# Kernel optimization log

Hardware: AMD Instinct MI355X
Metric: run time of the kernel (lower is better)

The kernel has to match this reference:

```python
import jax, jax.numpy as jnp
import numpy as np

N_HEADS = 8
N_LSTM_LAYERS = 32
HID = 25  # LSTM hidden units == decoder seq_len
EPS = 1e-5


def _layernorm(x, g, b):
    m = x.mean(-1, keepdims=True)
    v = x.var(-1, keepdims=True)  # biased, as torch LayerNorm
    return (x - m) / jnp.sqrt(v + EPS) * g + b


def _mha(q_in, k_in, v_in, Wq, bq, Wk, bk, Wv, bv, Wo, bo):
    B, L, D = q_in.shape
    S = k_in.shape[1]
    E = D // N_HEADS
    q = (q_in @ Wq + bq).reshape(B, L, N_HEADS, E)
    k = (k_in @ Wk + bk).reshape(B, S, N_HEADS, E)
    v = (v_in @ Wv + bv).reshape(B, S, N_HEADS, E)
    scores = jnp.einsum('blhe,bshe->bhls', q, k) / jnp.sqrt(jnp.asarray(E, q.dtype))
    attn = jax.nn.softmax(scores, axis=-1)
    out = jnp.einsum('bhls,bshe->blhe', attn, v).reshape(B, L, D)
    return out @ Wo + bo


def _lstm_layer(inp, W_ih, W_hh, b_ih, b_hh):
    # inp: [B, T, F]; PyTorch gate order i, f, g, o
    B = inp.shape[0]
    h0 = jnp.zeros((B, HID), inp.dtype)
    c0 = jnp.zeros((B, HID), inp.dtype)
    bias = b_ih + b_hh

    def step(carry, x_t):
        h, c = carry
        gates = x_t @ W_ih.T + h @ W_hh.T + bias  # [B, 4H]
        i, f, g, o = jnp.split(gates, 4, axis=-1)
        c = jax.nn.sigmoid(f) * c + jax.nn.sigmoid(i) * jnp.tanh(g)
        h = jax.nn.sigmoid(o) * jnp.tanh(c)
        return (h, c), h

    xs = jnp.swapaxes(inp, 0, 1)  # [T, B, F]
    _, hs = jax.lax.scan(step, (h0, c0), xs)
    return jnp.swapaxes(hs, 0, 1)  # [B, T, H]


def _forward(x, cross,
             Wq_s, bq_s, Wk_s, bk_s, Wv_s, bv_s, Wo_s, bo_s,
             Wq_c, bq_c, Wk_c, bk_c, Wv_c, bv_c, Wo_c, bo_c,
             g1, b1, g2, b2, g3, b3,
             W_ih, W_hh, b_ih, b_hh, Wc, bc):
    x = x + _mha(x, x, x, Wq_s, bq_s, Wk_s, bk_s, Wv_s, bv_s, Wo_s, bo_s)
    x = _layernorm(x, g1, b1)
    x = x + _mha(x, cross, cross, Wq_c, bq_c, Wk_c, bk_c, Wv_c, bv_c, Wo_c, bo_c)
    x = _layernorm(x, g2, b2)
    # LSTM runs over the feature axis: [B, L=25, D=512] -> [B, T=512, F=25]
    y = jnp.swapaxes(x, 1, 2)
    for l in range(N_LSTM_LAYERS):
        y = _lstm_layer(y, W_ih[l], W_hh[l], b_ih[l], b_hh[l])
    # pointwise conv over channels (dim 1 of [B, 512, 25])
    final_y = jnp.einsum('oc,bcl->bol', Wc, y) + bc[None, :, None]
    final_y = jnp.swapaxes(final_y, 1, 2)  # [B, 25, 512]
    return _layernorm(x + final_y, g3, b3)


def setup_inputs() -> dict:
    key = jax.random.key(0)
    ks = jax.random.split(key, 24)
    B, L, S, D = 128, 25, 96, 512

    def rn(k, shape, scale=0.02):
        return jax.random.normal(k, shape, jnp.float32) * scale

    inp = {
        'x': jax.random.normal(ks[0], (B, L, D), jnp.float32),
        'cross': jax.random.normal(ks[1], (B, S, D), jnp.float32),
        'Wq_s': rn(ks[2], (D, D)), 'bq_s': jnp.zeros(D),
        'Wk_s': rn(ks[3], (D, D)), 'bk_s': jnp.zeros(D),
        'Wv_s': rn(ks[4], (D, D)), 'bv_s': jnp.zeros(D),
        'Wo_s': rn(ks[5], (D, D)), 'bo_s': jnp.zeros(D),
        'Wq_c': rn(ks[6], (D, D)), 'bq_c': jnp.zeros(D),
        'Wk_c': rn(ks[7], (D, D)), 'bk_c': jnp.zeros(D),
        'Wv_c': rn(ks[8], (D, D)), 'bv_c': jnp.zeros(D),
        'Wo_c': rn(ks[9], (D, D)), 'bo_c': jnp.zeros(D),
        'g1': jnp.ones(D), 'b1': jnp.zeros(D),
        'g2': jnp.ones(D), 'b2': jnp.zeros(D),
        'g3': jnp.ones(D), 'b3': jnp.zeros(D),
        'W_ih': rn(ks[10], (N_LSTM_LAYERS, 4 * HID, HID), 0.1),
        'W_hh': rn(ks[11], (N_LSTM_LAYERS, 4 * HID, HID), 0.1),
        'b_ih': jnp.zeros((N_LSTM_LAYERS, 4 * HID)),
        'b_hh': jnp.zeros((N_LSTM_LAYERS, 4 * HID)),
        'Wc': rn(ks[12], (D, D)), 'bc': jnp.zeros(D),
    }
    return inp


def reference(x, cross,
              Wq_s, bq_s, Wk_s, bk_s, Wv_s, bv_s, Wo_s, bo_s,
              Wq_c, bq_c, Wk_c, bk_c, Wv_c, bv_c, Wo_c, bo_c,
              g1, b1, g2, b2, g3, b3,
              W_ih, W_hh, b_ih, b_hh, Wc, bc):
    return _forward(x, cross,
                    Wq_s, bq_s, Wk_s, bk_s, Wv_s, bv_s, Wo_s, bo_s,
                    Wq_c, bq_c, Wk_c, bk_c, Wv_c, bv_c, Wo_c, bo_c,
                    g1, b1, g2, b2, g3, b3,
                    W_ih, W_hh, b_ih, b_hh, Wc, bc)
```

## Files before the change

### kernel.cpp

```cpp
#include <hip/hip_runtime.h>


#define EPS_LN 1e-5f

typedef _Float16 h2v __attribute__((ext_vector_type(2)));
typedef _Float16 h8v __attribute__((ext_vector_type(8)));
typedef float    f4v __attribute__((ext_vector_type(4)));

#if defined(__has_builtin)
#if __has_builtin(__builtin_amdgcn_fdot2)
#define HAVE_FDOT2 1
#endif
#if __has_builtin(__builtin_amdgcn_rcpf)
#define HAVE_RCPF 1
#endif
#endif

__device__ __forceinline__ float fdot2(h2v a, h2v b, float c) {
#ifdef HAVE_FDOT2
  return __builtin_amdgcn_fdot2(a, b, c, false);
#else
  return c + (float)a.x * (float)b.x + (float)a.y * (float)b.y;
#endif
}
__device__ __forceinline__ h2v bch2(unsigned int u) {
  return __builtin_bit_cast(h2v, u);
}
__device__ __forceinline__ float rcp_fast(float x) {
#ifdef HAVE_RCPF
  return __builtin_amdgcn_rcpf(x);
#else
  return 1.f / x;
#endif
}
__device__ __forceinline__ float sigm_fast(float x) {
  return rcp_fast(1.f + __expf(-x));
}
__device__ __forceinline__ float tanh_fast(float x) {
  return 1.f - 2.f * rcp_fast(1.f + __expf(2.f * x));
}

struct WPtrs { const float* p[9]; };

__global__ __launch_bounds__(256)
void prep_weights(WPtrs w, _Float16* __restrict__ dst) {
  __shared__ float tile[32][33];
  const int z = blockIdx.z;
  const int tx = threadIdx.x & 31, ty = threadIdx.x >> 5;
  const int bx = blockIdx.x, by = blockIdx.y;
  const float* in = w.p[z];
  _Float16* outp = dst + (size_t)z * 262144;
  if (z < 8) {
#pragma unroll
    for (int i = 0; i < 4; i++)
      tile[ty + i * 8][tx] = in[(size_t)(by * 32 + ty + i * 8) * 512 + bx * 32 + tx];
    __syncthreads();
#pragma unroll
    for (int i = 0; i < 4; i++)
      outp[(size_t)(bx * 32 + ty + i * 8) * 512 + by * 32 + tx] = (_Float16)tile[tx][ty + i * 8];
  } else {
#pragma unroll
    for (int i = 0; i < 4; i++) {
      size_t off = (size_t)(by * 32 + ty + i * 8) * 512 + bx * 32 + tx;
      outp[off] = (_Float16)in[off];
    }
  }
}

__global__ __launch_bounds__(256)
void gemm3(const float* __restrict__ A,
           const _Float16* __restrict__ BT0, const _Float16* __restrict__ BT1,
           const _Float16* __restrict__ BT2,
           const float* __restrict__ bias0, const float* __restrict__ bias1,
           const float* __restrict__ bias2,
           float* __restrict__ C0, float* __restrict__ C1, float* __restrict__ C2,
           int M) {
  __shared__ _Float16 Asld[64 * 40];
  __shared__ _Float16 Bsld[64 * 40];
  const int t = threadIdx.x;
  const int which = blockIdx.x >> 3;
  const int n0 = (blockIdx.x & 7) * 64;
  const int m0 = blockIdx.y * 64;
  const _Float16* BT = (which == 0) ? BT0 : (which == 1) ? BT1 : BT2;
  const float* bias  = (which == 0) ? bias0 : (which == 1) ? bias1 : bias2;
  float* C           = (which == 0) ? C0 : (which == 1) ? C1 : C2;

  const int r = t >> 2, q = t & 3;
  const int w = t >> 6;
  const int lane = t & 63;
  const int lm = lane & 15, q8 = lane >> 4;

  f4v acc[4] = {};
  for (int k0 = 0; k0 < 512; k0 += 32) {
    __syncthreads();
    float4 f0 = *(const float4*)&A[(size_t)(m0 + r) * 512 + k0 + q * 8];
    float4 f1 = *(const float4*)&A[(size_t)(m0 + r) * 512 + k0 + q * 8 + 4];
    h8v hvv = {(_Float16)f0.x, (_Float16)f0.y, (_Float16)f0.z, (_Float16)f0.w,
               (_Float16)f1.x, (_Float16)f1.y, (_Float16)f1.z, (_Float16)f1.w};
    *(h8v*)&Asld[r * 40 + q * 8] = hvv;
    *(uint4*)&Bsld[r * 40 + q * 8] = *(const uint4*)&BT[(size_t)(n0 + r) * 512 + k0 + q * 8];
    __syncthreads();
    h8v a = *(const h8v*)&Asld[(w * 16 + lm) * 40 + q8 * 8];
#pragma unroll
    for (int nt = 0; nt < 4; nt++) {
      h8v b = *(const h8v*)&Bsld[(nt * 16 + lm) * 40 + q8 * 8];
      acc[nt] = __builtin_amdgcn_mfma_f32_16x16x32_f16(a, b, acc[nt], 0, 0, 0);
    }
  }
#pragma unroll
  for (int nt = 0; nt < 4; nt++) {
    int gn = n0 + nt * 16 + lm;
    float bv = bias[gn];
#pragma unroll
    for (int rg = 0; rg < 4; rg++) {
      int gm = m0 + w * 16 + q8 * 4 + rg;
      C[(size_t)gm * 512 + gn] = acc[nt][rg] + bv;
    }
  }
}

template <int S>
__global__ __launch_bounds__(256)
void attn_scores(const float* __restrict__ Q, const float* __restrict__ K,
                 float* __restrict__ P) {
  __shared__ float Qs[25][64];
  __shared__ float Ks[S][65];
  const int h = blockIdx.x, b = blockIdx.y, t = threadIdx.x;
  for (int idx = t; idx < 25 * 64; idx += 256) {
    int l = idx >> 6, e = idx & 63;
    Qs[l][e] = Q[(b * 25 + l) * 512 + h * 64 + e];
  }
  for (int idx = t; idx < S * 64; idx += 256) {
    int s = idx >> 6, e = idx & 63;
    Ks[s][e] = K[(b * S + s) * 512 + h * 64 + e];
  }
  __syncthreads();
  float* Pb = P + (size_t)(b * 8 + h) * 25 * S;
  for (int idx = t; idx < 25 * S; idx += 256) {
    int l = idx / S, s = idx % S;
    float acc = 0.f;
#pragma unroll
    for (int e = 0; e < 64; e++) acc += Qs[l][e] * Ks[s][e];
    Pb[idx] = acc * 0.125f;
  }
}

template <int S>
__global__ __launch_bounds__(256)
void attn_out(const float* __restrict__ P, const float* __restrict__ V,
              float* __restrict__ O) {
  __shared__ float Ps[25][S];
  __shared__ float Vs[S][64];
  const int h = blockIdx.x, b = blockIdx.y, t = threadIdx.x;
  const float* Pb = P + (size_t)(b * 8 + h) * 25 * S;
  for (int idx = t; idx < 25 * S; idx += 256) Ps[idx / S][idx % S] = Pb[idx];
  for (int idx = t; idx < S * 64; idx += 256) {
    int s = idx >> 6, e = idx & 63;
    Vs[s][e] = V[(b * S + s) * 512 + h * 64 + e];
  }
  __syncthreads();
  if (t < 25) {
    float mx = -1e30f;
    for (int s = 0; s < S; s++) mx = fmaxf(mx, Ps[t][s]);
    float sum = 0.f;
    for (int s = 0; s < S; s++) { float p = __expf(Ps[t][s] - mx); Ps[t][s] = p; sum += p; }
    float r = 1.f / sum;
    for (int s = 0; s < S; s++) Ps[t][s] *= r;
  }
  __syncthreads();
  for (int idx = t; idx < 25 * 64; idx += 256) {
    int l = idx >> 6, e = idx & 63;
    float acc = 0.f;
    for (int s = 0; s < S; s++) acc += Ps[l][s] * Vs[s][e];
    O[(b * 25 + l) * 512 + h * 64 + e] = acc;
  }
}

__global__ __launch_bounds__(128)
void add_ln(const float* __restrict__ a, const float* __restrict__ b,
            const float* __restrict__ gw, const float* __restrict__ bw,
            float* __restrict__ out) {
  const int row = blockIdx.x, t = threadIdx.x;
  float4 va = ((const float4*)(a + (size_t)row * 512))[t];
  float4 vb = ((const float4*)(b + (size_t)row * 512))[t];
  float4 v = make_float4(va.x + vb.x, va.y + vb.y, va.z + vb.z, va.w + vb.w);
  float s = v.x + v.y + v.z + v.w;
  float q = v.x * v.x + v.y * v.y + v.z * v.z + v.w * v.w;
#pragma unroll
  for (int off = 32; off > 0; off >>= 1) {
    s += __shfl_down(s, off);
    q += __shfl_down(q, off);
  }
  __shared__ float red[4];
  if ((t & 63) == 0) { red[(t >> 6) * 2] = s; red[(t >> 6) * 2 + 1] = q; }
  __syncthreads();
  float S_ = red[0] + red[2], Q_ = red[1] + red[3];
  float mean = S_ * (1.f / 512.f);
  float var  = Q_ * (1.f / 512.f) - mean * mean;
  float inv  = rsqrtf(var + EPS_LN);
  float4 g4 = ((const float4*)gw)[t];
  float4 b4 = ((const float4*)bw)[t];
  float4 o;
  o.x = (v.x - mean) * inv * g4.x + b4.x;
  o.y = (v.y - mean) * inv * g4.y + b4.y;
  o.z = (v.z - mean) * inv * g4.z + b4.z;
  o.w = (v.w - mean) * inv * g4.w + b4.w;
  ((float4*)(out + (size_t)row * 512))[t] = o;
}

__global__ void transpose_dl(const float* __restrict__ in, float* __restrict__ outp) {
  const int b = blockIdx.x, t = threadIdx.x;
  for (int idx = t; idx < 25 * 512; idx += 256) {
    int l2 = idx / 512, c = idx % 512;
    outp[((size_t)b * 25 + l2) * 512 + c] = in[((size_t)b * 512 + c) * 25 + l2];
  }
}

__global__ __launch_bounds__(256)
void prep_x0r(const float* __restrict__ x2, _Float16* __restrict__ X0) {
  __shared__ float tile[25][516];
  const int b = blockIdx.x, t = threadIdx.x;
  for (int idx = t; idx < 25 * 512; idx += 256) {
    int u = idx >> 9, d = idx & 511;
    tile[u][d] = x2[((size_t)b * 25 + u) * 512 + d];
  }
  __syncthreads();
  for (int idx = t; idx < 512 * 32; idx += 256) {
    int d = idx >> 5, u = idx & 31;
    X0[((size_t)b * 512 + d) * 32 + u] = (u < 25) ? (_Float16)tile[u][d] : (_Float16)0.f;
  }
}

#define NLAY 32
#define NGRP 16
#define BGRP 8
#define NPIPE 64
#define CHT  8
#define NCHK 64
#define RSLOTS 64
#define RCHK (RSLOTS / CHT)
#define RLAY ((size_t)128 * RSLOTS * 32)

__device__ __forceinline__ int ld_rlx(int* p) {
  return __hip_atomic_load(p, __ATOMIC_RELAXED, __HIP_MEMORY_SCOPE_AGENT);
}
__device__ __forceinline__ void st_rlx(int* p, int v) {
  __hip_atomic_store(p, v, __ATOMIC_RELAXED, __HIP_MEMORY_SCOPE_AGENT);
}
__device__ __forceinline__ unsigned long long ldq_rlx(const unsigned long long* p) {
  return __hip_atomic_load(p, __ATOMIC_RELAXED, __HIP_MEMORY_SCOPE_AGENT);
}
__device__ __forceinline__ void sth_rlx(_Float16* p, _Float16 v) {
  __hip_atomic_store((unsigned short*)p, __builtin_bit_cast(unsigned short, v),
                     __ATOMIC_RELAXED, __HIP_MEMORY_SCOPE_AGENT);
}

__global__ __launch_bounds__(256) __attribute__((amdgpu_waves_per_eu(2, 2)))
void lstm_pipeline(const _Float16* __restrict__ X0, float* __restrict__ yout,
                   _Float16* __restrict__ ring, int* __restrict__ prod,
                   int* __restrict__ cons,
                   const float* __restrict__ Wih, const float* __restrict__ Whh,
                   const float* __restrict__ bih, const float* __restrict__ bhh) {
  const int l = blockIdx.x / NGRP;
  const int g = blockIdx.x % NGRP;
  const int t = threadIdx.x;
  const int lane = t & 63;
  const int wv = t >> 6;
  const int u  = t & 31;
  const int bi = t >> 5;
  const int p  = g * 4 + wv;
  const bool active = (u < 25);

  __shared__ _Float16 xbuf[CHT][BGRP][32];
  __shared__ _Float16 hbuf[BGRP][32];

  h2v wih2[4][13], whh2[4][13];
  float bias_r[4];
  float c_reg = 0.f;
  {
    const int uc = active ? u : 24;
#pragma unroll
    for (int j = 0; j < 4; j++) {
      const float* wi = &Wih[((size_t)l * 100 + j * 25 + uc) * 25];
      const float* wh = &Whh[((size_t)l * 100 + j * 25 + uc) * 25];
#pragma unroll
      for (int k = 0; k < 13; k++) {
        float alo = wi[2 * k], ahi = (2 * k + 1 < 25) ? wi[2 * k + 1] : 0.f;
        float blo = wh[2 * k], bhi = (2 * k + 1 < 25) ? wh[2 * k + 1] : 0.f;
        wih2[j][k] = h2v{(_Float16)alo, (_Float16)ahi};
        whh2[j][k] = h2v{(_Float16)blo, (_Float16)bhi};
      }
      bias_r[j] = bih[l * 100 + j * 25 + uc] + bhh[l * 100 + j * 25 + uc];
    }
  }
  hbuf[2 * wv + (lane >> 5)][lane & 31] = (_Float16)0.f;

  _Float16* ring_out = ring + (size_t)l * RLAY
                       + ((size_t)(g * BGRP + bi) * RSLOTS) * 32 + u;
  float* yout_out = yout + ((size_t)(g * BGRP + bi) * 512) * 25 + u;

  const int s_tc = lane >> 3;
  const int s_b2 = 2 * wv + ((lane >> 2) & 1);
  const int s_seg = lane & 3;

  int* prod_in   = prod + (l - 1) * NPIPE + p;
  int* prod_out  = prod + l * NPIPE + p;
  int* cons_self = cons + l * NPIPE + p;
  int* cons_up   = cons + (l + 1) * NPIPE + p;

  for (int n = 0; n < NCHK; n++) {
    if (l > 0) {
      while (ld_rlx(prod_in) < n + 1) __builtin_amdgcn_s_sleep(1);
    }
    if (l < NLAY - 1 && n >= RCHK) {
      while (ld_rlx(cons_up) < n - RCHK + 1) __builtin_amdgcn_s_sleep(1);
    }
    asm volatile("" ::: "memory");

    {
      const int tg = n * CHT + s_tc;
      if (l == 0) {
        const uint4* p4 = (const uint4*)(X0
            + (((size_t)(g * BGRP + s_b2) * 512) + tg) * 32 + s_seg * 8);
        *(uint4*)&xbuf[s_tc][s_b2][s_seg * 8] = *p4;
      } else {
        const unsigned long long* p8 = (const unsigned long long*)(ring
            + (size_t)(l - 1) * RLAY
            + (((size_t)(g * BGRP + s_b2) * RSLOTS) + (tg & (RSLOTS - 1))) * 32
            + s_seg * 8);
        unsigned long long a = ldq_rlx(p8);
        unsigned long long b = ldq_rlx(p8 + 1);
        *(uint4*)&xbuf[s_tc][s_b2][s_seg * 8] =
            make_uint4((unsigned)a, (unsigned)(a >> 32),
                       (unsigned)b, (unsigned)(b >> 32));
      }
    }
    asm volatile("s_waitcnt lgkmcnt(0)" ::: "memory");
    if (lane == 0 && l > 0) st_rlx(cons_self, n + 1);

    float ax[CHT][4];
    if (active) {
#pragma unroll
      for (int tc = 0; tc < CHT; tc++) {
        const unsigned int* xr = (const unsigned int*)&xbuf[tc][bi][0];
        uint4 xa = *(const uint4*)(xr);
        uint4 xb = *(const uint4*)(xr + 4);
        uint4 xc = *(const uint4*)(xr + 8);
        unsigned int xd = xr[12];
        h2v xk[13] = {bch2(xa.x), bch2(xa.y), bch2(xa.z), bch2(xa.w),
                      bch2(xb.x), bch2(xb.y), bch2(xb.z), bch2(xb.w),
                      bch2(xc.x), bch2(xc.y), bch2(xc.z), bch2(xc.w),
                      bch2(xd)};
        float a0 = bias_r[0], a1 = bias_r[1], a2 = bias_r[2], a3 = bias_r[3];
#pragma unroll
        for (int k = 0; k < 13; k++) {
          a0 = fdot2(wih2[0][k], xk[k], a0);
          a1 = fdot2(wih2[1][k], xk[k], a1);
          a2 = fdot2(wih2[2][k], xk[k], a2);
          a3 = fdot2(wih2[3][k], xk[k], a3);
        }
        ax[tc][0] = a0; ax[tc][1] = a1; ax[tc][2] = a2; ax[tc][3] = a3;
      }
    }

#pragma unroll
    for (int tc = 0; tc < CHT; tc++) {
      const int tg = n * CHT + tc;
      if (active) {
        const unsigned int* hr = (const unsigned int*)&hbuf[bi][0];
        uint4 ha = *(const uint4*)(hr);
        uint4 hb = *(const uint4*)(hr + 4);
        uint4 hc = *(const uint4*)(hr + 8);
        unsigned int hd = hr[12];
        h2v hk[13] = {bch2(ha.x), bch2(ha.y), bch2(ha.z), bch2(ha.w),
                      bch2(hb.x), bch2(hb.y), bch2(hb.z), bch2(hb.w),
                      bch2(hc.x), bch2(hc.y), bch2(hc.z), bch2(hc.w),
                      bch2(hd)};
        float a0 = ax[tc][0], a1 = ax[tc][1], a2 = ax[tc][2], a3 = ax[tc][3];
#pragma unroll
        for (int k = 0; k < 13; k++) {
          a0 = fdot2(whh2[0][k], hk[k], a0);
          a1 = fdot2(whh2[1][k], hk[k], a1);
          a2 = fdot2(whh2[2][k], hk[k], a2);
          a3 = fdot2(whh2[3][k], hk[k], a3);
        }
        float si = sigm_fast(a0);
        float sf = sigm_fast(a1);
        float so = sigm_fast(a3);
        c_reg = sf * c_reg + si * tanh_fast(a2);
        float h = so * tanh_fast(c_reg);
        _Float16 h16 = (_Float16)h;
        hbuf[bi][u] = h16;
        if (l == NLAY - 1)
          yout_out[(size_t)tg * 25] = h;
        else
          sth_rlx(ring_out + (size_t)(tg & (RSLOTS - 1)) * 32, h16);
      }
    }
    asm volatile("s_waitcnt vmcnt(0)" ::: "memory");
    if (lane == 0 && l < NLAY - 1) st_rlx(prod_out, n + 1);
  }
}

extern "C" void kernel_launch(void* const* d_in, const int* in_sizes, int n_in,
                              void* d_out, int out_size, void* d_ws, size_t ws_size,
                              hipStream_t stream) {
  const float* x     = (const float*)d_in[0];
  const float* cross = (const float*)d_in[1];
  const float* Wq_s = (const float*)d_in[2];  const float* bq_s = (const float*)d_in[3];
  const float* Wk_s = (const float*)d_in[4];  const float* bk_s = (const float*)d_in[5];
  const float* Wv_s = (const float*)d_in[6];  const float* bv_s = (const float*)d_in[7];
  const float* Wo_s = (const float*)d_in[8];  const float* bo_s = (const float*)d_in[9];
  const float* Wq_c = (const float*)d_in[10]; const float* bq_c = (const float*)d_in[11];
  const float* Wk_c = (const float*)d_in[12]; const float* bk_c = (const float*)d_in[13];
  const float* Wv_c = (const float*)d_in[14]; const float* bv_c = (const float*)d_in[15];
  const float* Wo_c = (const float*)d_in[16]; const float* bo_c = (const float*)d_in[17];
  const float* g1 = (const float*)d_in[18]; const float* b1 = (const float*)d_in[19];
  const float* g2 = (const float*)d_in[20]; const float* b2 = (const float*)d_in[21];
  const float* g3 = (const float*)d_in[22]; const float* b3 = (const float*)d_in[23];
  const float* Wih = (const float*)d_in[24];
  const float* Whh = (const float*)d_in[25];
  const float* bih = (const float*)d_in[26];
  const float* bhh = (const float*)d_in[27];
  const float* Wc  = (const float*)d_in[28]; const float* bc = (const float*)d_in[29];
  float* out = (float*)d_out;
  float* ws  = (float*)d_ws;

  constexpr size_t A  = 1638400;
  constexpr size_t C6 = 6291456;
  float* x1    = ws;
  float* Qc    = ws + A;
  float* Qs    = ws + 2 * A;
  float* Ks    = ws + 3 * A;
  float* Vs    = ws + 4 * A;
  float* attns = ws + 5 * A;
  float* tmp   = ws + 6 * A;
  float* Ps    = ws + 7 * A;
  float* Kc    = ws + 2 * A;
  float* Vc    = ws + 2 * A + C6;
  float* attnc = ws + 2 * A + 2 * C6;
  float* Pc    = attnc + A;
  float* tmp2  = ws + 6 * A;
  float* x2    = ws + 3 * A;
  _Float16* X0b  = (_Float16*)(ws + 4 * A);
  float*    youtb = ws + 5 * A;
  _Float16* ringb = (_Float16*)(ws + 6 * A);
  float* ytb   = ws + 2 * A;
  float* fy    = ws + 5 * A;
  _Float16* WTall = (_Float16*)(ws + 20000000);
  int* ctr = (int*)(ws + 21179648);

  dim3 blk(256);
  WPtrs wpq;
  wpq.p[0] = Wq_s; wpq.p[1] = Wk_s; wpq.p[2] = Wv_s; wpq.p[3] = Wo_s;
  wpq.p[4] = Wq_c; wpq.p[5] = Wk_c; wpq.p[6] = Wv_c; wpq.p[7] = Wo_c;
  wpq.p[8] = Wc;
  prep_weights<<<dim3(16, 16, 9), blk, 0, stream>>>(wpq, WTall);
  hipMemsetAsync(ctr, 0, 4096 * sizeof(int), stream);
  _Float16* WT[9];
  for (int i = 0; i < 9; i++) WT[i] = WTall + (size_t)i * 262144;

  gemm3<<<dim3(24, 50), blk, 0, stream>>>(x, WT[0], WT[1], WT[2],
                                          bq_s, bk_s, bv_s, Qs, Ks, Vs, 3200);
  attn_scores<25><<<dim3(8, 128), blk, 0, stream>>>(Qs, Ks, Ps);
  attn_out<25><<<dim3(8, 128), blk, 0, stream>>>(Ps, Vs, attns);
  gemm3<<<dim3(8, 50), blk, 0, stream>>>(attns, WT[3], WT[3], WT[3],
                                         bo_s, bo_s, bo_s, tmp, tmp, tmp, 3200);
  add_ln<<<3200, 128, 0, stream>>>(x, tmp, g1, b1, x1);
  gemm3<<<dim3(8, 50), blk, 0, stream>>>(x1, WT[4], WT[4], WT[4],
                                         bq_c, bq_c, bq_c, Qc, Qc, Qc, 3200);
  gemm3<<<dim3(16, 192), blk, 0, stream>>>(cross, WT[5], WT[6], WT[6],
                                           bk_c, bv_c, bv_c, Kc, Vc, Vc, 12288);
  attn_scores<96><<<dim3(8, 128), blk, 0, stream>>>(Qc, Kc, Pc);
  attn_out<96><<<dim3(8, 128), blk, 0, stream>>>(Pc, Vc, attnc);
  gemm3<<<dim3(8, 50), blk, 0, stream>>>(attnc, WT[7], WT[7], WT[7],
                                         bo_c, bo_c, bo_c, tmp2, tmp2, tmp2, 3200);
  add_ln<<<3200, 128, 0, stream>>>(x1, tmp2, g2, b2, x2);
  prep_x0r<<<128, 256, 0, stream>>>(x2, X0b);
  lstm_pipeline<<<NLAY * NGRP, 256, 0, stream>>>(X0b, youtb, ringb, ctr, ctr + 2048,
                                                 Wih, Whh, bih, bhh);
  transpose_dl<<<128, 256, 0, stream>>>(youtb, ytb);
  gemm3<<<dim3(8, 50), blk, 0, stream>>>(ytb, WT[8], WT[8], WT[8],
                                         bc, bc, bc, fy, fy, fy, 3200);
  add_ln<<<3200, 128, 0, stream>>>(x2, fy, g3, b3, out);
}
```

Measured before the change: 912.3 us.

## Remap LSTM pipeline so a block's waves hold consecutive layers, handing off via LDS

Each block of the layer-pipelined LSTM used to hold one layer for 8 batch rows, with every layer-to-layer handoff going through a global ring buffer and agent-scope atomic counters. Now each block holds 4 consecutive layers (one per wave) for 2 batch rows. Inside a block, hidden states pass through an LDS ring with LDS producer/consumer counters, so global ring traffic and global polling only happen at boundaries between blocks of 4 layers. This cuts global memory latency on the pipeline's critical path. In exchange it adds intra-block spin-waiting on LDS counters and a 4-slot LDS buffer that could stall waves.

```diff
diff --git a/kernel.cpp b/kernel.cpp
--- a/kernel.cpp
+++ b/kernel.cpp
@@ -232,11 +232,12 @@
 }
 
 #define NLAY 32
-#define NGRP 16
-#define BGRP 8
+#define LGRP 8
+#define WPB  4
 #define NPIPE 64
 #define CHT  8
 #define NCHK 64
+#define NSLOT 4
 #define RSLOTS 64
 #define RCHK (RSLOTS / CHT)
 #define RLAY ((size_t)128 * RSLOTS * 32)
@@ -253,6 +254,12 @@
 __device__ __forceinline__ void sth_rlx(_Float16* p, _Float16 v) {
   __hip_atomic_store((unsigned short*)p, __builtin_bit_cast(unsigned short, v),
                      __ATOMIC_RELAXED, __HIP_MEMORY_SCOPE_AGENT);
+}
+__device__ __forceinline__ int ld_lds(int* p) {
+  return __hip_atomic_load(p, __ATOMIC_RELAXED, __HIP_MEMORY_SCOPE_WORKGROUP);
+}
+__device__ __forceinline__ void st_lds(int* p, int v) {
+  __hip_atomic_store(p, v, __ATOMIC_RELAXED, __HIP_MEMORY_SCOPE_WORKGROUP);
 }
 
 __global__ __launch_bounds__(256) __attribute__((amdgpu_waves_per_eu(2, 2)))
@@ -261,18 +268,29 @@
                    int* __restrict__ cons,
                    const float* __restrict__ Wih, const float* __restrict__ Whh,
                    const float* __restrict__ bih, const float* __restrict__ bhh) {
-  const int l = blockIdx.x / NGRP;
-  const int g = blockIdx.x % NGRP;
+  const int lg = blockIdx.x / NPIPE;
+  const int p  = blockIdx.x % NPIPE;
   const int t = threadIdx.x;
   const int lane = t & 63;
   const int wv = t >> 6;
-  const int u  = t & 31;
-  const int bi = t >> 5;
-  const int p  = g * 4 + wv;
+  const int l  = lg * WPB + wv;
+  const int u  = lane & 31;
+  const int bi = lane >> 5;
   const bool active = (u < 25);
 
-  __shared__ _Float16 xbuf[CHT][BGRP][32];
-  __shared__ _Float16 hbuf[BGRP][32];
+  __shared__ _Float16 lbuf[3][NSLOT][CHT][2][32];
+  __shared__ _Float16 inbuf[CHT][2][32];
+  __shared__ _Float16 hbuf[WPB][2][32];
+  __shared__ int lprod[3], lcons[3];
+
+  for (int idx = t; idx < 3 * NSLOT * CHT * 2 * 32; idx += 256)
+    ((_Float16*)lbuf)[idx] = (_Float16)0.f;
+  for (int idx = t; idx < CHT * 2 * 32; idx += 256)
+    ((_Float16*)inbuf)[idx] = (_Float16)0.f;
+  for (int idx = t; idx < WPB * 2 * 32; idx += 256)
+    ((_Float16*)hbuf)[idx] = (_Float16)0.f;
+  if (t < 3) { lprod[t] = 0; lcons[t] = 0; }
+  __syncthreads();
 
   h2v wih2[4][13], whh2[4][13];
   float bias_r[4];
@@ -293,56 +311,64 @@
       bias_r[j] = bih[l * 100 + j * 25 + uc] + bhh[l * 100 + j * 25 + uc];
     }
   }
-  hbuf[2 * wv + (lane >> 5)][lane & 31] = (_Float16)0.f;
-
-  _Float16* ring_out = ring + (size_t)l * RLAY
-                       + ((size_t)(g * BGRP + bi) * RSLOTS) * 32 + u;
-  float* yout_out = yout + ((size_t)(g * BGRP + bi) * 512) * 25 + u;
-
-  const int s_tc = lane >> 3;
-  const int s_b2 = 2 * wv + ((lane >> 2) & 1);
-  const int s_seg = lane & 3;
-
-  int* prod_in   = prod + (l - 1) * NPIPE + p;
-  int* prod_out  = prod + l * NPIPE + p;
-  int* cons_self = cons + l * NPIPE + p;
-  int* cons_up   = cons + (l + 1) * NPIPE + p;
+
+  const int gb = p * 2 + bi;
+  _Float16* ring_out = ring + (size_t)l * RLAY + ((size_t)gb * RSLOTS) * 32 + u;
+  float* yout_out = yout + ((size_t)gb * 512) * 25 + u;
+
+  const int s_tc = lane >> 3, s_half = (lane >> 2) & 1, s_seg = lane & 3;
+  const int s_gb = p * 2 + s_half;
+
+  int* gprod_in  = prod + (lg - 1) * NPIPE + p;
+  int* gcons_in  = cons + (lg - 1) * NPIPE + p;
+  int* gprod_out = prod + lg * NPIPE + p;
+  int* gcons_out = cons + lg * NPIPE + p;
 
   for (int n = 0; n < NCHK; n++) {
-    if (l > 0) {
-      while (ld_rlx(prod_in) < n + 1) __builtin_amdgcn_s_sleep(1);
-    }
-    if (l < NLAY - 1 && n >= RCHK) {
-      while (ld_rlx(cons_up) < n - RCHK + 1) __builtin_amdgcn_s_sleep(1);
+    const int slot = n & (NSLOT - 1);
+    if (wv == 0) {
+      if (lg > 0) {
+        while (ld_rlx(gprod_in) < n + 1) __builtin_amdgcn_s_sleep(1);
+      }
+    } else {
+      while (ld_lds(&lprod[wv - 1]) < n + 1) __builtin_amdgcn_s_sleep(1);
+    }
+    if (wv < 3) {
+      if (n >= NSLOT) {
+        while (ld_lds(&lcons[wv]) < n - NSLOT + 1) __builtin_amdgcn_s_sleep(1);
+      }
+    } else if (lg < LGRP - 1 && n >= RCHK) {
+      while (ld_rlx(gcons_out) < n - RCHK + 1) __builtin_amdgcn_s_sleep(1);
     }
     asm volatile("" ::: "memory");
 
-    {
+    if (wv == 0) {
       const int tg = n * CHT + s_tc;
-      if (l == 0) {
+      if (lg == 0) {
         const uint4* p4 = (const uint4*)(X0
-            + (((size_t)(g * BGRP + s_b2) * 512) + tg) * 32 + s_seg * 8);
-        *(uint4*)&xbuf[s_tc][s_b2][s_seg * 8] = *p4;
+            + (((size_t)s_gb * 512) + tg) * 32 + s_seg * 8);
+        *(uint4*)&inbuf[s_tc][s_half][s_seg * 8] = *p4;
       } else {
         const unsigned long long* p8 = (const unsigned long long*)(ring
             + (size_t)(l - 1) * RLAY
-            + (((size_t)(g * BGRP + s_b2) * RSLOTS) + (tg & (RSLOTS - 1))) * 32
-            + s_seg * 8);
+            + (((size_t)s_gb * RSLOTS) + (tg & (RSLOTS - 1))) * 32 + s_seg * 8);
         unsigned long long a = ldq_rlx(p8);
         unsigned long long b = ldq_rlx(p8 + 1);
-        *(uint4*)&xbuf[s_tc][s_b2][s_seg * 8] =
+        *(uint4*)&inbuf[s_tc][s_half][s_seg * 8] =
             make_uint4((unsigned)a, (unsigned)(a >> 32),
                        (unsigned)b, (unsigned)(b >> 32));
       }
-    }
-    asm volatile("s_waitcnt lgkmcnt(0)" ::: "memory");
-    if (lane == 0 && l > 0) st_rlx(cons_self, n + 1);
-
+      asm volatile("s_waitcnt lgkmcnt(0)" ::: "memory");
+      if (lg > 0 && lane == 0) st_rlx(gcons_in, n + 1);
+    }
+
+    const _Float16* xbase = (wv == 0) ? &inbuf[0][0][0]
+                                      : &lbuf[wv - 1][slot][0][0][0];
     float ax[CHT][4];
     if (active) {
 #pragma unroll
       for (int tc = 0; tc < CHT; tc++) {
-        const unsigned int* xr = (const unsigned int*)&xbuf[tc][bi][0];
+        const unsigned int* xr = (const unsigned int*)(xbase + (tc * 2 + bi) * 32);
         uint4 xa = *(const uint4*)(xr);
         uint4 xb = *(const uint4*)(xr + 4);
         uint4 xc = *(const uint4*)(xr + 8);
@@ -362,12 +388,14 @@
         ax[tc][0] = a0; ax[tc][1] = a1; ax[tc][2] = a2; ax[tc][3] = a3;
       }
     }
+    asm volatile("s_waitcnt lgkmcnt(0)" ::: "memory");
+    if (wv > 0 && lane == 0) st_lds(&lcons[wv - 1], n + 1);
 
 #pragma unroll
     for (int tc = 0; tc < CHT; tc++) {
       const int tg = n * CHT + tc;
       if (active) {
-        const unsigned int* hr = (const unsigned int*)&hbuf[bi][0];
+        const unsigned int* hr = (const unsigned int*)&hbuf[wv][bi][0];
         uint4 ha = *(const uint4*)(hr);
         uint4 hb = *(const uint4*)(hr + 4);
         uint4 hc = *(const uint4*)(hr + 8);
@@ -390,15 +418,23 @@
         c_reg = sf * c_reg + si * tanh_fast(a2);
         float h = so * tanh_fast(c_reg);
         _Float16 h16 = (_Float16)h;
-        hbuf[bi][u] = h16;
-        if (l == NLAY - 1)
+        hbuf[wv][bi][u] = h16;
+        if (wv < 3) {
+          lbuf[wv][slot][tc][bi][u] = h16;
+        } else if (l == NLAY - 1) {
           yout_out[(size_t)tg * 25] = h;
-        else
+        } else {
           sth_rlx(ring_out + (size_t)(tg & (RSLOTS - 1)) * 32, h16);
+        }
       }
     }
-    asm volatile("s_waitcnt vmcnt(0)" ::: "memory");
-    if (lane == 0 && l < NLAY - 1) st_rlx(prod_out, n + 1);
+    if (wv < 3) {
+      asm volatile("s_waitcnt lgkmcnt(0)" ::: "memory");
+      if (lane == 0) st_lds(&lprod[wv], n + 1);
+    } else {
+      asm volatile("s_waitcnt vmcnt(0)" ::: "memory");
+      if (lg < LGRP - 1 && lane == 0) st_rlx(gprod_out, n + 1);
+    }
   }
 }
 
@@ -477,8 +513,8 @@
                                          bo_c, bo_c, bo_c, tmp2, tmp2, tmp2, 3200);
   add_ln<<<3200, 128, 0, stream>>>(x1, tmp2, g2, b2, x2);
   prep_x0r<<<128, 256, 0, stream>>>(x2, X0b);
-  lstm_pipeline<<<NLAY * NGRP, 256, 0, stream>>>(X0b, youtb, ringb, ctr, ctr + 2048,
-                                                 Wih, Whh, bih, bhh);
+  lstm_pipeline<<<LGRP * NPIPE, 256, 0, stream>>>(X0b, youtb, ringb, ctr, ctr + 2048,
+                                                  Wih, Whh, bih, bhh);
   transpose_dl<<<128, 256, 0, stream>>>(youtb, ytb);
   gemm3<<<dim3(8, 50), blk, 0, stream>>>(ytb, WT[8], WT[8], WT[8],
                                          bc, bc, bc, fy, fy, fy, 3200);
```

After: 845.2 us (median of 3 runs). 1.08x faster.
